# Performance work log

Hardware: AMD Instinct MI355X
Metric: run time of the kernel (lower is better)

## Reference

```python
import jax, jax.numpy as jnp
import numpy as np

N_NODES = 50000
N_EDGES = 800000
D = 128
N_REL = 4
N_GRAPHS = 128
N_CLASSES = 16


def rgcn_layer(x, W_rel, W_root, b, src, dst, edge_type):
    # Per-relation transform of all nodes: [N, R, D]
    xt = jnp.einsum('nd,rdf->nrf', x, W_rel)
    msg = xt[src, edge_type]  # [E, D] gather message per edge
    # mean aggregation per (dst, relation) pair (PyG RGCNConv aggr='mean')
    seg = dst * N_REL + edge_type
    cnt = jax.ops.segment_sum(jnp.ones((src.shape[0],), x.dtype), seg,
                              num_segments=N_NODES * N_REL)
    norm = 1.0 / jnp.maximum(cnt[seg], 1.0)
    agg = jax.ops.segment_sum(msg * norm[:, None], dst, num_segments=N_NODES)
    return agg + x @ W_root + b


def setup_inputs() -> dict:
    key = jax.random.key(0)
    ks = jax.random.split(key, 12)
    s = 1.0 / np.sqrt(D)
    inp = {
        'x': jax.random.normal(ks[0], (N_NODES, D), jnp.float32),
        'edge_index': jax.random.randint(ks[1], (2, N_EDGES), 0, N_NODES, jnp.int64),
        'edge_type': jax.random.randint(ks[2], (N_EDGES,), 0, N_REL, jnp.int64),
        'batch': jnp.sort(jax.random.randint(ks[3], (N_NODES,), 0, N_GRAPHS, jnp.int64)),
        'W_rel1': jax.random.normal(ks[4], (N_REL, D, D), jnp.float32) * s,
        'W_root1': jax.random.normal(ks[5], (D, D), jnp.float32) * s,
        'b1': jnp.zeros((D,), jnp.float32),
        'W_rel2': jax.random.normal(ks[6], (N_REL, D, D), jnp.float32) * s,
        'W_root2': jax.random.normal(ks[7], (D, D), jnp.float32) * s,
        'b2': jnp.zeros((D,), jnp.float32),
        'W_cls': jax.random.normal(ks[8], (D, N_CLASSES), jnp.float32) * s,
        'b_cls': jnp.zeros((N_CLASSES,), jnp.float32),
    }
    return inp


def reference(x, edge_index, edge_type, batch, W_rel1, W_root1, b1,
              W_rel2, W_root2, b2, W_cls, b_cls):
    src, dst = edge_index[0], edge_index[1]
    h = jax.nn.relu(rgcn_layer(x, W_rel1, W_root1, b1, src, dst, edge_type))
    h = jax.nn.relu(rgcn_layer(h, W_rel2, W_root2, b2, src, dst, edge_type))
    # global mean pool over graphs (dropout is identity: training=False)
    gsum = jax.ops.segment_sum(h, batch, num_segments=N_GRAPHS)
    gcnt = jax.ops.segment_sum(jnp.ones((h.shape[0],), h.dtype), batch,
                               num_segments=N_GRAPHS)
    g = gsum / jnp.maximum(gcnt, 1.0)[:, None]
    return g @ W_cls + b_cls
```

## Files before the change

### kernel.cpp

```cpp
#include <hip/hip_runtime.h>

#define D_DIM 128
#define N_REL 4
#define CAP 32

typedef __attribute__((ext_vector_type(8))) short bf16x8;
typedef __attribute__((ext_vector_type(4))) float f32x4;

static inline int cdiv(int a, int b) { return (a + b - 1) / b; }

__device__ inline ushort f2bf(float f) {
    union { float f; unsigned u; } v;
    v.f = f;
    unsigned r = v.u + 0x7FFFu + ((v.u >> 16) & 1u);
    return (ushort)(r >> 16);
}

__device__ inline float bf2f(ushort u) {
    union { unsigned u; float f; } v;
    v.u = (unsigned)u << 16;
    return v.f;
}

__device__ inline float uif(unsigned u) {
    union { unsigned u; float f; } v;
    v.u = u;
    return v.f;
}

#define CNT_B 391
#define CAST_B 782
#define CAST_FULL 781
#define PACK_B 80

__global__ __launch_bounds__(256) void prep_kernel(
    const float* __restrict__ x, ushort* __restrict__ Xb,
    const int* __restrict__ src, const int* __restrict__ dst,
    const int* __restrict__ et, unsigned* __restrict__ icnt,
    ushort* __restrict__ esorted,
    const float* __restrict__ Wrel1, const float* __restrict__ Wroot1,
    const float* __restrict__ Wrel2, const float* __restrict__ Wroot2,
    ushort* __restrict__ Wpk1, ushort* __restrict__ Wpk2,
    int n4, int nEdges) {
    int b = blockIdx.x;
    if (b < CNT_B) {
        int e = (b * 256 + threadIdx.x) * 8;
        if (e >= nEdges) return;
        if (e + 8 <= nEdges) {
            int4 sA = *(const int4*)(src + e);
            int4 sB = *(const int4*)(src + e + 4);
            int4 dA = *(const int4*)(dst + e);
            int4 dB = *(const int4*)(dst + e + 4);
            int4 tA = *(const int4*)(et + e);
            int4 tB = *(const int4*)(et + e + 4);
            unsigned o0 = atomicAdd(&icnt[dA.x], 1u << (8 * tA.x));
            unsigned o1 = atomicAdd(&icnt[dA.y], 1u << (8 * tA.y));
            unsigned o2 = atomicAdd(&icnt[dA.z], 1u << (8 * tA.z));
            unsigned o3 = atomicAdd(&icnt[dA.w], 1u << (8 * tA.w));
            unsigned o4 = atomicAdd(&icnt[dB.x], 1u << (8 * tB.x));
            unsigned o5 = atomicAdd(&icnt[dB.y], 1u << (8 * tB.y));
            unsigned o6 = atomicAdd(&icnt[dB.z], 1u << (8 * tB.z));
            unsigned o7 = atomicAdd(&icnt[dB.w], 1u << (8 * tB.w));
            int r0 = (int)(((o0 >> (8 * tA.x)) & 0xFFu) - 0xAAu);
            int r1 = (int)(((o1 >> (8 * tA.y)) & 0xFFu) - 0xAAu);
            int r2 = (int)(((o2 >> (8 * tA.z)) & 0xFFu) - 0xAAu);
            int r3 = (int)(((o3 >> (8 * tA.w)) & 0xFFu) - 0xAAu);
            int r4 = (int)(((o4 >> (8 * tB.x)) & 0xFFu) - 0xAAu);
            int r5 = (int)(((o5 >> (8 * tB.y)) & 0xFFu) - 0xAAu);
            int r6 = (int)(((o6 >> (8 * tB.z)) & 0xFFu) - 0xAAu);
            int r7 = (int)(((o7 >> (8 * tB.w)) & 0xFFu) - 0xAAu);
            esorted[((size_t)(dA.x * N_REL + tA.x) << 5) + r0] = (ushort)sA.x;
            esorted[((size_t)(dA.y * N_REL + tA.y) << 5) + r1] = (ushort)sA.y;
            esorted[((size_t)(dA.z * N_REL + tA.z) << 5) + r2] = (ushort)sA.z;
            esorted[((size_t)(dA.w * N_REL + tA.w) << 5) + r3] = (ushort)sA.w;
            esorted[((size_t)(dB.x * N_REL + tB.x) << 5) + r4] = (ushort)sB.x;
            esorted[((size_t)(dB.y * N_REL + tB.y) << 5) + r5] = (ushort)sB.y;
            esorted[((size_t)(dB.z * N_REL + tB.z) << 5) + r6] = (ushort)sB.z;
            esorted[((size_t)(dB.w * N_REL + tB.w) << 5) + r7] = (ushort)sB.w;
        } else {
            for (int j = 0; e + j < nEdges; ++j) {
                int dd = dst[e + j], tt = et[e + j];
                unsigned o = atomicAdd(&icnt[dd], 1u << (8 * tt));
                int r = (int)(((o >> (8 * tt)) & 0xFFu) - 0xAAu);
                esorted[((size_t)(dd * N_REL + tt) << 5) + r] = (ushort)src[e + j];
            }
        }
    } else if (b < CNT_B + CAST_B) {
        int rb = b - CNT_B;
        int base = rb * 2048 + threadIdx.x;
        if (rb < CAST_FULL) {
            float4 v0 = ((const float4*)x)[base];
            float4 v1 = ((const float4*)x)[base + 256];
            float4 v2 = ((const float4*)x)[base + 512];
            float4 v3 = ((const float4*)x)[base + 768];
            float4 v4 = ((const float4*)x)[base + 1024];
            float4 v5 = ((const float4*)x)[base + 1280];
            float4 v6 = ((const float4*)x)[base + 1536];
            float4 v7 = ((const float4*)x)[base + 1792];
            ushort4 o0, o1, o2, o3, o4, o5, o6, o7;
            o0.x = f2bf(v0.x); o0.y = f2bf(v0.y); o0.z = f2bf(v0.z); o0.w = f2bf(v0.w);
            o1.x = f2bf(v1.x); o1.y = f2bf(v1.y); o1.z = f2bf(v1.z); o1.w = f2bf(v1.w);
            o2.x = f2bf(v2.x); o2.y = f2bf(v2.y); o2.z = f2bf(v2.z); o2.w = f2bf(v2.w);
            o3.x = f2bf(v3.x); o3.y = f2bf(v3.y); o3.z = f2bf(v3.z); o3.w = f2bf(v3.w);
            o4.x = f2bf(v4.x); o4.y = f2bf(v4.y); o4.z = f2bf(v4.z); o4.w = f2bf(v4.w);
            o5.x = f2bf(v5.x); o5.y = f2bf(v5.y); o5.z = f2bf(v5.z); o5.w = f2bf(v5.w);
            o6.x = f2bf(v6.x); o6.y = f2bf(v6.y); o6.z = f2bf(v6.z); o6.w = f2bf(v6.w);
            o7.x = f2bf(v7.x); o7.y = f2bf(v7.y); o7.z = f2bf(v7.z); o7.w = f2bf(v7.w);
            ((ushort4*)Xb)[base] = o0;
            ((ushort4*)Xb)[base + 256] = o1;
            ((ushort4*)Xb)[base + 512] = o2;
            ((ushort4*)Xb)[base + 768] = o3;
            ((ushort4*)Xb)[base + 1024] = o4;
            ((ushort4*)Xb)[base + 1280] = o5;
            ((ushort4*)Xb)[base + 1536] = o6;
            ((ushort4*)Xb)[base + 1792] = o7;
        } else {
#pragma unroll
            for (int j = 0; j < 8; ++j) {
                int i = base + j * 256;
                if (i < n4) {
                    float4 v = ((const float4*)x)[i];
                    ushort4 o;
                    o.x = f2bf(v.x); o.y = f2bf(v.y); o.z = f2bf(v.z); o.w = f2bf(v.w);
                    ((ushort4*)Xb)[i] = o;
                }
            }
        }
    } else {
        int pb = b - (CNT_B + CAST_B);
        int layer = pb / 40;
        int rem = pb % 40;
        int mat = rem >> 3;
        int blk = rem & 7;
        const float* Wrel = layer ? Wrel2 : Wrel1;
        const float* Wroot = layer ? Wroot2 : Wroot1;
        ushort* out = layer ? Wpk2 : Wpk1;
        const float* W = (mat < N_REL) ? (Wrel + (size_t)mat * D_DIM * D_DIM) : Wroot;
        int t = blk * 256 + threadIdx.x;
        int lane = t & 63;
        int tile = t >> 6;
        int kt = tile >> 3;
        int nt = tile & 7;
        int n = nt * 16 + (lane & 15);
        int kb = kt * 32 + (lane >> 4) * 8;
        ushort* o = out + (((size_t)mat * 32 + tile) * 64 + lane) * 8;
        ushort4 lo, hi;
        lo.x = f2bf(W[(kb + 0) * D_DIM + n]);
        lo.y = f2bf(W[(kb + 1) * D_DIM + n]);
        lo.z = f2bf(W[(kb + 2) * D_DIM + n]);
        lo.w = f2bf(W[(kb + 3) * D_DIM + n]);
        hi.x = f2bf(W[(kb + 4) * D_DIM + n]);
        hi.y = f2bf(W[(kb + 5) * D_DIM + n]);
        hi.z = f2bf(W[(kb + 6) * D_DIM + n]);
        hi.w = f2bf(W[(kb + 7) * D_DIM + n]);
        *(ushort4*)(o) = lo;
        *(ushort4*)(o + 4) = hi;
    }
}

__global__ __launch_bounds__(256) void sort_kernel(
    const unsigned* __restrict__ icnt, ushort* __restrict__ esorted, int nseg) {
    __shared__ int ids[16][34];
    __shared__ int sids[16][34];
    const int tid = threadIdx.x;
    const int ql = tid & 15;
    const int qd = tid >> 4;
    const int seg0 = blockIdx.x * 64;

    unsigned cwv[4], idwv[4];
#pragma unroll
    for (int p = 0; p < 4; ++p) {
        int seg = seg0 + p * 16 + qd;
        if (seg < nseg) {
            cwv[p] = icnt[seg >> 2];
            idwv[p] = ((const unsigned*)(esorted + ((size_t)seg << 5)))[ql];
        } else {
            cwv[p] = 0xAAAAAAAAu;
            idwv[p] = 0u;
        }
    }

    for (int p = 0; p < 4; ++p) {
        int seg = seg0 + p * 16 + qd;
        if (seg >= nseg) continue;
        int deg = (int)(((cwv[p] >> ((seg & 3) * 8)) & 0xFFu) - 0xAAu);
        if (deg < 2) continue;
        ids[qd][2 * ql] = (int)(idwv[p] & 0xFFFFu);
        ids[qd][2 * ql + 1] = (int)(idwv[p] >> 16);
        __threadfence_block();
#pragma unroll
        for (int base = 0; base < 2; ++base) {
            int j = base * 16 + ql;
            if (j < deg) {
                int v = ids[qd][j];
                int rank = 0;
                int k = 0;
                for (; k + 4 <= deg; k += 4) {
                    int w0 = ids[qd][k], w1 = ids[qd][k + 1];
                    int w2 = ids[qd][k + 2], w3 = ids[qd][k + 3];
                    rank += (w0 < v || (w0 == v && k < j)) ? 1 : 0;
                    rank += (w1 < v || (w1 == v && k + 1 < j)) ? 1 : 0;
                    rank += (w2 < v || (w2 == v && k + 2 < j)) ? 1 : 0;
                    rank += (w3 < v || (w3 == v && k + 3 < j)) ? 1 : 0;
                }
                for (; k < deg; ++k) {
                    int wv = ids[qd][k];
                    rank += (wv < v || (wv == v && k < j)) ? 1 : 0;
                }
                sids[qd][rank] = v;
            }
        }
        __threadfence_block();
        ushort* row = esorted + ((size_t)seg << 5);
        for (int j = ql; j < deg; j += 16) row[j] = (ushort)sids[qd][j];
        __threadfence_block();
    }
}

__global__ __launch_bounds__(256, 6) void layer_kernel(
    const ushort* __restrict__ Xb, const unsigned* __restrict__ icnt,
    const ushort* __restrict__ esorted, const ushort* __restrict__ Wpk,
    const float* __restrict__ bias, ushort* __restrict__ outb, int n_nodes) {
    __shared__ ushort Ms[16][520];
    __shared__ unsigned idsU[16][4][17];
    const int tid = threadIdx.x;
    const int wave = tid >> 6;
    const int lane = tid & 63;
    const int ql = tid & 15;
    const int qd = tid >> 4;
    const int m = lane & 15;
    const int q = lane >> 4;
    const int r0 = blockIdx.x * 16;
    const int rel = qd & 3;
    const int rowgrp = qd >> 2;

    unsigned cw4[4];
#pragma unroll
    for (int p = 0; p < 4; ++p) {
        int node = r0 + p * 4 + rowgrp;
        int vnode = min(node, n_nodes - 1);
        cw4[p] = (node < n_nodes) ? icnt[vnode] : 0xAAAAAAAAu;
        unsigned idw = ((const unsigned*)(esorted +
                        (((size_t)vnode * N_REL + rel) << 5)))[ql];
        idsU[qd][p][ql] = idw;
    }
    __threadfence_block();

    auto acc8 = [](float* a, uint4 u) {
        a[0] += uif(u.x << 16); a[1] += uif(u.x & 0xFFFF0000u);
        a[2] += uif(u.y << 16); a[3] += uif(u.y & 0xFFFF0000u);
        a[4] += uif(u.z << 16); a[5] += uif(u.z & 0xFFFF0000u);
        a[6] += uif(u.w << 16); a[7] += uif(u.w & 0xFFFF0000u);
    };

    const ushort* xb = Xb + ql * 8;
#pragma unroll
    for (int p = 0; p < 4; ++p) {
        const int row = p * 4 + rowgrp;
        const int deg = (int)(((cw4[p] >> (rel * 8)) & 0xFFu) - 0xAAu);
        uint4* mrow = (uint4*)&Ms[row][rel * 128 + ql * 8];
        if (deg <= 0) {
            *mrow = make_uint4(0u, 0u, 0u, 0u);
            continue;
        }
        const unsigned* idp = idsU[qd][p];
        float a[8], b[8];
#pragma unroll
        for (int j = 0; j < 8; ++j) { a[j] = 0.f; b[j] = 0.f; }
        int e = 0;
        for (; e + 4 <= deg; e += 4) {
            unsigned w0 = idp[e >> 1];
            unsigned w1 = idp[(e >> 1) + 1];
            size_t s0 = (size_t)(w0 & 0xFFFFu) * D_DIM;
            size_t s1 = (size_t)(w0 >> 16) * D_DIM;
            size_t s2 = (size_t)(w1 & 0xFFFFu) * D_DIM;
            size_t s3 = (size_t)(w1 >> 16) * D_DIM;
            uint4 u0 = *(const uint4*)(xb + s0);
            uint4 u1 = *(const uint4*)(xb + s1);
            uint4 u2 = *(const uint4*)(xb + s2);
            uint4 u3 = *(const uint4*)(xb + s3);
            acc8(a, u0); acc8(b, u1); acc8(a, u2); acc8(b, u3);
        }
        if (e + 2 <= deg) {
            unsigned w0 = idp[e >> 1];
            size_t s0 = (size_t)(w0 & 0xFFFFu) * D_DIM;
            size_t s1 = (size_t)(w0 >> 16) * D_DIM;
            uint4 u0 = *(const uint4*)(xb + s0);
            uint4 u1 = *(const uint4*)(xb + s1);
            acc8(a, u0); acc8(b, u1);
            e += 2;
        }
        if (e < deg) {
            size_t s0 = (size_t)(idp[e >> 1] & 0xFFFFu) * D_DIM;
            uint4 u0 = *(const uint4*)(xb + s0);
            acc8(a, u0);
        }
        float sc = 1.0f / (float)deg;
        uint4 o;
        o.x = (unsigned)f2bf((a[0] + b[0]) * sc) | ((unsigned)f2bf((a[1] + b[1]) * sc) << 16);
        o.y = (unsigned)f2bf((a[2] + b[2]) * sc) | ((unsigned)f2bf((a[3] + b[3]) * sc) << 16);
        o.z = (unsigned)f2bf((a[4] + b[4]) * sc) | ((unsigned)f2bf((a[5] + b[5]) * sc) << 16);
        o.w = (unsigned)f2bf((a[6] + b[6]) * sc) | ((unsigned)f2bf((a[7] + b[7]) * sc) << 16);
        *mrow = o;
    }
    __syncthreads();

    f32x4 acc0 = (f32x4){0.f, 0.f, 0.f, 0.f};
    f32x4 acc1 = (f32x4){0.f, 0.f, 0.f, 0.f};
#pragma unroll
    for (int ph = 0; ph < N_REL; ++ph) {
#pragma unroll
        for (int kt = 0; kt < 4; ++kt) {
            bf16x8 a = *(const bf16x8*)&Ms[m][ph * 128 + kt * 32 + q * 8];
            bf16x8 b0 = *(const bf16x8*)(Wpk + (((size_t)ph * 32 + kt * 8 + wave * 2) * 64 + lane) * 8);
            bf16x8 b1 = *(const bf16x8*)(Wpk + (((size_t)ph * 32 + kt * 8 + wave * 2 + 1) * 64 + lane) * 8);
            acc0 = __builtin_amdgcn_mfma_f32_16x16x32_bf16(a, b0, acc0, 0, 0, 0);
            acc1 = __builtin_amdgcn_mfma_f32_16x16x32_bf16(a, b1, acc1, 0, 0, 0);
        }
    }
    {
        const int n0 = min(r0 + m, n_nodes - 1);
        const ushort* aX = Xb + (size_t)n0 * D_DIM + q * 8;
#pragma unroll
        for (int kt = 0; kt < 4; ++kt) {
            bf16x8 a = *(const bf16x8*)(aX + kt * 32);
            bf16x8 b0 = *(const bf16x8*)(Wpk + (((size_t)N_REL * 32 + kt * 8 + wave * 2) * 64 + lane) * 8);
            bf16x8 b1 = *(const bf16x8*)(Wpk + (((size_t)N_REL * 32 + kt * 8 + wave * 2 + 1) * 64 + lane) * 8);
            acc0 = __builtin_amdgcn_mfma_f32_16x16x32_bf16(a, b0, acc0, 0, 0, 0);
            acc1 = __builtin_amdgcn_mfma_f32_16x16x32_bf16(a, b1, acc1, 0, 0, 0);
        }
    }

#pragma unroll
    for (int j = 0; j < 2; ++j) {
        const f32x4 av = j ? acc1 : acc0;
        int col = (wave * 2 + j) * 16 + m;
        float bv = bias[col];
#pragma unroll
        for (int r = 0; r < 4; ++r) {
            int orow = r0 + q * 4 + r;
            if (orow < n_nodes)
                outb[(size_t)orow * D_DIM + col] = f2bf(fmaxf(av[r] + bv, 0.0f));
        }
    }
}

__global__ __launch_bounds__(1024) void poolcls_kernel(
    const ushort* __restrict__ hb, const int* __restrict__ batch,
    const float* __restrict__ Wcls, const float* __restrict__ bcls,
    float* __restrict__ out, int n_nodes) {
    __shared__ float part[64][D_DIM + 1];
    __shared__ float mean[D_DIM];
    __shared__ float cpart[16][17];
    int g = blockIdx.x;
    int tid = threadIdx.x;
    int par = tid >> 4;
    int dg = (tid & 15) * 8;
    auto lb = [&](int val) {
        int lo = 0, hi = n_nodes;
        while (lo < hi) {
            int mid = (lo + hi) >> 1;
            if (batch[mid] < val) lo = mid + 1; else hi = mid;
        }
        return lo;
    };
    int lo = lb(g), hi = lb(g + 1);
    float a[8];
#pragma unroll
    for (int j = 0; j < 8; ++j) a[j] = 0.f;
    for (int nn = lo + par; nn < hi; nn += 64) {
        uint4 u = *(const uint4*)(hb + (size_t)nn * D_DIM + dg);
        a[0] += uif(u.x << 16); a[1] += uif(u.x & 0xFFFF0000u);
        a[2] += uif(u.y << 16); a[3] += uif(u.y & 0xFFFF0000u);
        a[4] += uif(u.z << 16); a[5] += uif(u.z & 0xFFFF0000u);
        a[6] += uif(u.w << 16); a[7] += uif(u.w & 0xFFFF0000u);
    }
#pragma unroll
    for (int j = 0; j < 8; ++j) part[par][dg + j] = a[j];
    __syncthreads();
    if (tid < D_DIM) {
        float s = 0.f;
#pragma unroll
        for (int j = 0; j < 64; ++j) s += part[j][tid];
        mean[tid] = s / fmaxf((float)(hi - lo), 1.0f);
    }
    __syncthreads();
    if (tid < 256) {
        int c = tid & 15, kc = tid >> 4;
        float s = 0.f;
#pragma unroll
        for (int j = 0; j < 8; ++j)
            s = fmaf(mean[kc * 8 + j], Wcls[(kc * 8 + j) * 16 + c], s);
        cpart[kc][c] = s;
    }
    __syncthreads();
    if (tid < 16) {
        float s = bcls[tid];
#pragma unroll
        for (int k = 0; k < 16; ++k) s += cpart[k][tid];
        out[g * 16 + tid] = s;
    }
}

extern "C" void kernel_launch(void* const* d_in, const int* in_sizes, int n_in,
                              void* d_out, int out_size, void* d_ws, size_t ws_size,
                              hipStream_t stream) {
    const float* x      = (const float*)d_in[0];
    const int*   ei     = (const int*)d_in[1];
    const int*   etype  = (const int*)d_in[2];
    const int*   batch  = (const int*)d_in[3];
    const float* Wrel1  = (const float*)d_in[4];
    const float* Wroot1 = (const float*)d_in[5];
    const float* b1     = (const float*)d_in[6];
    const float* Wrel2  = (const float*)d_in[7];
    const float* Wroot2 = (const float*)d_in[8];
    const float* b2     = (const float*)d_in[9];
    const float* Wcls   = (const float*)d_in[10];
    const float* bcls   = (const float*)d_in[11];
    float* out = (float*)d_out;

    const int N = in_sizes[0] / D_DIM;
    const int E = in_sizes[1] / 2;
    const int NSEG = N * N_REL;
    const int* src = ei;
    const int* dst = ei + E;

    ushort* Xb   = (ushort*)d_ws;
    ushort* h1b  = Xb + (size_t)N * D_DIM;
    ushort* h2b  = h1b + (size_t)N * D_DIM;
    ushort* Wpk1 = h2b + (size_t)N * D_DIM;
    ushort* Wpk2 = Wpk1 + 81920;
    unsigned* icnt = (unsigned*)(Wpk2 + 81920);
    ushort* esorted = (ushort*)(icnt + N);

    prep_kernel<<<CNT_B + CAST_B + PACK_B, 256, 0, stream>>>(
        x, Xb, src, dst, etype, icnt, esorted, Wrel1, Wroot1, Wrel2, Wroot2,
        Wpk1, Wpk2, N * D_DIM / 4, E);

    sort_kernel<<<cdiv(NSEG, 64), 256, 0, stream>>>(icnt, esorted, NSEG);

    layer_kernel<<<cdiv(N, 16), 256, 0, stream>>>(
        Xb, icnt, esorted, Wpk1, b1, h1b, N);

    layer_kernel<<<cdiv(N, 16), 256, 0, stream>>>(
        h1b, icnt, esorted, Wpk2, b2, h2b, N);

    poolcls_kernel<<<128, 1024, 0, stream>>>(h2b, batch, Wcls, bcls, out, N);
}
```

Baseline: 256.1 us.

## Fuse per-segment neighbor sort into first layer kernel

Removes the standalone sort kernel and performs the rank-based sort of each (node, relation) neighbor list inside the first layer kernel, using the ids already staged in shared memory. The sorted ids are used directly from shared memory for the gather in layer 1 and written back to global memory for layer 2, which is specialised through a template flag to skip sorting. This saves one launch plus a separate read/write pass over the edge lists, but adds sort compute and extra shared memory to the first layer kernel, which may lower its occupancy.

```diff
diff --git a/kernel.cpp b/kernel.cpp
--- a/kernel.cpp
+++ b/kernel.cpp
@@ -158,71 +158,14 @@
     }
 }
 
-__global__ __launch_bounds__(256) void sort_kernel(
-    const unsigned* __restrict__ icnt, ushort* __restrict__ esorted, int nseg) {
-    __shared__ int ids[16][34];
-    __shared__ int sids[16][34];
-    const int tid = threadIdx.x;
-    const int ql = tid & 15;
-    const int qd = tid >> 4;
-    const int seg0 = blockIdx.x * 64;
-
-    unsigned cwv[4], idwv[4];
-#pragma unroll
-    for (int p = 0; p < 4; ++p) {
-        int seg = seg0 + p * 16 + qd;
-        if (seg < nseg) {
-            cwv[p] = icnt[seg >> 2];
-            idwv[p] = ((const unsigned*)(esorted + ((size_t)seg << 5)))[ql];
-        } else {
-            cwv[p] = 0xAAAAAAAAu;
-            idwv[p] = 0u;
-        }
-    }
-
-    for (int p = 0; p < 4; ++p) {
-        int seg = seg0 + p * 16 + qd;
-        if (seg >= nseg) continue;
-        int deg = (int)(((cwv[p] >> ((seg & 3) * 8)) & 0xFFu) - 0xAAu);
-        if (deg < 2) continue;
-        ids[qd][2 * ql] = (int)(idwv[p] & 0xFFFFu);
-        ids[qd][2 * ql + 1] = (int)(idwv[p] >> 16);
-        __threadfence_block();
-#pragma unroll
-        for (int base = 0; base < 2; ++base) {
-            int j = base * 16 + ql;
-            if (j < deg) {
-                int v = ids[qd][j];
-                int rank = 0;
-                int k = 0;
-                for (; k + 4 <= deg; k += 4) {
-                    int w0 = ids[qd][k], w1 = ids[qd][k + 1];
-                    int w2 = ids[qd][k + 2], w3 = ids[qd][k + 3];
-                    rank += (w0 < v || (w0 == v && k < j)) ? 1 : 0;
-                    rank += (w1 < v || (w1 == v && k + 1 < j)) ? 1 : 0;
-                    rank += (w2 < v || (w2 == v && k + 2 < j)) ? 1 : 0;
-                    rank += (w3 < v || (w3 == v && k + 3 < j)) ? 1 : 0;
-                }
-                for (; k < deg; ++k) {
-                    int wv = ids[qd][k];
-                    rank += (wv < v || (wv == v && k < j)) ? 1 : 0;
-                }
-                sids[qd][rank] = v;
-            }
-        }
-        __threadfence_block();
-        ushort* row = esorted + ((size_t)seg << 5);
-        for (int j = ql; j < deg; j += 16) row[j] = (ushort)sids[qd][j];
-        __threadfence_block();
-    }
-}
-
+template <bool DO_SORT>
 __global__ __launch_bounds__(256, 6) void layer_kernel(
     const ushort* __restrict__ Xb, const unsigned* __restrict__ icnt,
-    const ushort* __restrict__ esorted, const ushort* __restrict__ Wpk,
+    ushort* __restrict__ esorted, const ushort* __restrict__ Wpk,
     const float* __restrict__ bias, ushort* __restrict__ outb, int n_nodes) {
     __shared__ ushort Ms[16][520];
     __shared__ unsigned idsU[16][4][17];
+    __shared__ ushort sid16[DO_SORT ? 16 : 1][4][34];
     const int tid = threadIdx.x;
     const int wave = tid >> 6;
     const int lane = tid & 63;
@@ -246,6 +189,52 @@
     }
     __threadfence_block();
 
+    if constexpr (DO_SORT) {
+#pragma unroll
+        for (int p = 0; p < 4; ++p) {
+            const int deg = (int)(((cw4[p] >> (rel * 8)) & 0xFFu) - 0xAAu);
+            const unsigned* idp = idsU[qd][p];
+#pragma unroll
+            for (int base = 0; base < 2; ++base) {
+                int j = base * 16 + ql;
+                if (j < deg) {
+                    unsigned wj = idp[j >> 1];
+                    int v = (int)((j & 1) ? (wj >> 16) : (wj & 0xFFFFu));
+                    int rank = 0;
+                    int k = 0;
+                    for (; k + 4 <= deg; k += 4) {
+                        unsigned wa = idp[k >> 1];
+                        unsigned wb = idp[(k >> 1) + 1];
+                        int w0 = (int)(wa & 0xFFFFu), w1 = (int)(wa >> 16);
+                        int w2 = (int)(wb & 0xFFFFu), w3 = (int)(wb >> 16);
+                        rank += (w0 < v || (w0 == v && k < j)) ? 1 : 0;
+                        rank += (w1 < v || (w1 == v && k + 1 < j)) ? 1 : 0;
+                        rank += (w2 < v || (w2 == v && k + 2 < j)) ? 1 : 0;
+                        rank += (w3 < v || (w3 == v && k + 3 < j)) ? 1 : 0;
+                    }
+                    for (; k < deg; ++k) {
+                        unsigned wa = idp[k >> 1];
+                        int wv = (int)((k & 1) ? (wa >> 16) : (wa & 0xFFFFu));
+                        rank += (wv < v || (wv == v && k < j)) ? 1 : 0;
+                    }
+                    sid16[qd][p][rank] = (ushort)v;
+                }
+            }
+        }
+        __threadfence_block();
+#pragma unroll
+        for (int p = 0; p < 4; ++p) {
+            const int deg = (int)(((cw4[p] >> (rel * 8)) & 0xFFu) - 0xAAu);
+            if (deg >= 2 && 2 * ql < deg) {
+                int node = r0 + p * 4 + rowgrp;
+                unsigned* rowp = (unsigned*)(esorted +
+                                 (((size_t)node * N_REL + rel) << 5));
+                rowp[ql] = (unsigned)sid16[qd][p][2 * ql] |
+                           ((unsigned)sid16[qd][p][2 * ql + 1] << 16);
+            }
+        }
+    }
+
     auto acc8 = [](float* a, uint4 u) {
         a[0] += uif(u.x << 16); a[1] += uif(u.x & 0xFFFF0000u);
         a[2] += uif(u.y << 16); a[3] += uif(u.y & 0xFFFF0000u);
@@ -264,17 +253,23 @@
             continue;
         }
         const unsigned* idp = idsU[qd][p];
+        auto getid = [&](int e) -> size_t {
+            if constexpr (DO_SORT) {
+                return (size_t)sid16[qd][p][e] * D_DIM;
+            } else {
+                unsigned w = idp[e >> 1];
+                return (size_t)((e & 1) ? (w >> 16) : (w & 0xFFFFu)) * D_DIM;
+            }
+        };
         float a[8], b[8];
 #pragma unroll
         for (int j = 0; j < 8; ++j) { a[j] = 0.f; b[j] = 0.f; }
         int e = 0;
         for (; e + 4 <= deg; e += 4) {
-            unsigned w0 = idp[e >> 1];
-            unsigned w1 = idp[(e >> 1) + 1];
-            size_t s0 = (size_t)(w0 & 0xFFFFu) * D_DIM;
-            size_t s1 = (size_t)(w0 >> 16) * D_DIM;
-            size_t s2 = (size_t)(w1 & 0xFFFFu) * D_DIM;
-            size_t s3 = (size_t)(w1 >> 16) * D_DIM;
+            size_t s0 = getid(e);
+            size_t s1 = getid(e + 1);
+            size_t s2 = getid(e + 2);
+            size_t s3 = getid(e + 3);
             uint4 u0 = *(const uint4*)(xb + s0);
             uint4 u1 = *(const uint4*)(xb + s1);
             uint4 u2 = *(const uint4*)(xb + s2);
@@ -282,17 +277,15 @@
             acc8(a, u0); acc8(b, u1); acc8(a, u2); acc8(b, u3);
         }
         if (e + 2 <= deg) {
-            unsigned w0 = idp[e >> 1];
-            size_t s0 = (size_t)(w0 & 0xFFFFu) * D_DIM;
-            size_t s1 = (size_t)(w0 >> 16) * D_DIM;
+            size_t s0 = getid(e);
+            size_t s1 = getid(e + 1);
             uint4 u0 = *(const uint4*)(xb + s0);
             uint4 u1 = *(const uint4*)(xb + s1);
             acc8(a, u0); acc8(b, u1);
             e += 2;
         }
         if (e < deg) {
-            size_t s0 = (size_t)(idp[e >> 1] & 0xFFFFu) * D_DIM;
-            uint4 u0 = *(const uint4*)(xb + s0);
+            uint4 u0 = *(const uint4*)(xb + getid(e));
             acc8(a, u0);
         }
         float sc = 1.0f / (float)deg;
@@ -421,7 +414,6 @@
 
     const int N = in_sizes[0] / D_DIM;
     const int E = in_sizes[1] / 2;
-    const int NSEG = N * N_REL;
     const int* src = ei;
     const int* dst = ei + E;
 
@@ -437,12 +429,10 @@
         x, Xb, src, dst, etype, icnt, esorted, Wrel1, Wroot1, Wrel2, Wroot2,
         Wpk1, Wpk2, N * D_DIM / 4, E);
 
-    sort_kernel<<<cdiv(NSEG, 64), 256, 0, stream>>>(icnt, esorted, NSEG);
-
-    layer_kernel<<<cdiv(N, 16), 256, 0, stream>>>(
+    layer_kernel<true><<<cdiv(N, 16), 256, 0, stream>>>(
         Xb, icnt, esorted, Wpk1, b1, h1b, N);
 
-    layer_kernel<<<cdiv(N, 16), 256, 0, stream>>>(
+    layer_kernel<false><<<cdiv(N, 16), 256, 0, stream>>>(
         h1b, icnt, esorted, Wpk2, b2, h2b, N);
 
     poolcls_kernel<<<128, 1024, 0, stream>>>(h2b, batch, Wcls, bcls, out, N);
```

New measurement: 251.5 us. About the same (-1.8%).
